# Optimization experiments

Hardware: AMD Instinct MI355X
Metric: run time of the kernel (lower is better)

The kernel has to match this reference:

```python
import jax, jax.numpy as jnp
import numpy as np

EPS = 1e-6  # mmdet bbox_overlaps eps


def _nearest_bev(boxes7):
    # boxes7: [N, 7] = (x, y, z, dx, dy, dz, yaw). LiDARInstance3DBoxes.nearest_bev:
    # limit yaw to [-pi/2, pi/2) via limit_period(yaw, 0.5, pi); if |yaw| > pi/4 swap dx/dy,
    # then return axis-aligned (x1, y1, x2, y2).
    x, y = boxes7[:, 0], boxes7[:, 1]
    dx, dy = boxes7[:, 3], boxes7[:, 4]
    yaw = boxes7[:, 6]
    pi = jnp.float32(np.pi)
    normed = jnp.abs(yaw - jnp.floor(yaw / pi + 0.5) * pi)
    swap = normed > pi / 4
    w = jnp.where(swap, dy, dx)
    h = jnp.where(swap, dx, dy)
    return jnp.stack([x - w / 2, y - h / 2, x + w / 2, y + h / 2], axis=-1)


def _pairwise_iou(b):
    # b: [N, 4] x1y1x2y2 -> [N, N] IoU (mmdet bbox_overlaps, mode='iou')
    area = (b[:, 2] - b[:, 0]) * (b[:, 3] - b[:, 1])
    lt = jnp.maximum(b[:, None, :2], b[None, :, :2])
    rb = jnp.minimum(b[:, None, 2:], b[None, :, 2:])
    wh = jnp.clip(rb - lt, 0.0)
    inter = wh[..., 0] * wh[..., 1]
    union = jnp.maximum(area[:, None] + area[None, :] - inter, EPS)
    return inter / union


def setup_inputs() -> dict:
    key = jax.random.key(0)
    k1, k2, k3, k4, k5, k6 = jax.random.split(key, 6)
    B, A, C, H, W, box_dim = 2, 2, 10, 32, 32, 7
    N = H * W * A
    scores = jax.random.normal(k1, (B, A * C, H, W), jnp.float32)
    bbox_preds = jax.random.normal(k2, (B, A * box_dim, H, W), jnp.float32)
    pp_params = jax.random.normal(k3, (B, C * 3, H, W), jnp.float32)
    centers = jax.random.uniform(k4, (B, N, 3), jnp.float32, 0.0, 50.0)
    sizes = jax.random.uniform(k5, (B, N, 3), jnp.float32, 1.0, 5.0)
    yaw = jax.random.uniform(k6, (B, N, 1), jnp.float32, -np.pi, np.pi)
    decoded = jnp.concatenate([centers, sizes, yaw], axis=-1)  # [B, N, 7]
    return {"scores": scores, "bbox_preds": bbox_preds, "pp_params": pp_params, "decoded": decoded}


def reference(scores, bbox_preds, pp_params, decoded):
    B, AC, H, W = scores.shape
    N = decoded.shape[1]
    A = N // (H * W)
    C = AC // A
    # flatten_scores: (B,A,C,H,W) -> (B,H,W,A,C) -> (B, HWA, C)
    sc_f = scores.reshape(B, A, C, H, W).transpose(0, 3, 4, 1, 2).reshape(B, N, C)
    # flatten_pp: (B,C,3,H,W) -> (B,H,W,C,3), broadcast over A -> (B, HWA, C, 3)
    pp_hw = pp_params.reshape(B, C, 3, H, W).transpose(0, 3, 4, 1, 2)  # [B,H,W,C,3]
    pp_f = jnp.broadcast_to(pp_hw[:, :, :, None, :, :], (B, H, W, A, C, 3)).reshape(B, N, C, 3)
    # per-batch BEV IoU matrices
    bev = jax.vmap(_nearest_bev)(decoded[..., :7])        # [B, N, 4]
    iou = jax.vmap(_pairwise_iou)(bev)                    # [B, N, N]
    # per-class outer-product bias + row softmax + matmul with column softmax of scores
    p0 = pp_f[..., 0]                                     # [B, N, C]
    p1 = pp_f[..., 1]                                     # [B, N, C]
    bias = p0[:, :, None, :] * p1[:, None, :, :]          # [B, N, N, C]
    weight = jax.nn.softmax(iou[..., None] + bias, axis=2)  # softmax over keys (dim=1 of NxN)
    sm_sc = jax.nn.softmax(sc_f, axis=1)                  # softmax over N per class
    new_sc = jnp.einsum('bnmc,bmc->bnc', weight, sm_sc)   # [B, N, C]
    # un-flatten back to level layout: (B,H,W,A,C) -> (B, A*C, H, W)
    out_scores = new_sc.reshape(B, H, W, A, C).transpose(0, 3, 4, 1, 2).reshape(B, A * C, H, W)
    return out_scores, bbox_preds, pp_params
```

## Files before the change

### kernel.cpp

```cpp
#include <hip/hip_runtime.h>
#include <math.h>

#define Bz 2
#define Az 2
#define Cz 10
#define HWz 1024
#define Nz 2048
#define ACHW (Az*Cz*HWz)
#define NBBOX (Bz*Az*7*HWz)
#define NPP   (Bz*Cz*3*HWz)
#define EPSf 1e-6f
#define LOG2E 1.4426950408889634f

#if __has_builtin(__builtin_amdgcn_exp2f)
#define EXP2F(x) __builtin_amdgcn_exp2f(x)
#else
#define EXP2F(x) exp2f(x)
#endif
#if __has_builtin(__builtin_amdgcn_rcpf)
#define RCPF(x) __builtin_amdgcn_rcpf(x)
#else
#define RCPF(x) (1.0f/(x))
#endif

static __device__ __forceinline__ unsigned short f2bf(float x) {
    unsigned u = __builtin_bit_cast(unsigned, x);
    unsigned r = (u + 0x7fffu + ((u >> 16) & 1u)) >> 16;
    return (unsigned short)r;
}

#if __has_builtin(__builtin_amdgcn_update_dpp)
static __device__ __forceinline__ float wred(float x) {
    int t;
    t = __builtin_amdgcn_update_dpp(0, __builtin_bit_cast(int, x), 0x111, 0xf, 0xf, true);
    x += __builtin_bit_cast(float, t);
    t = __builtin_amdgcn_update_dpp(0, __builtin_bit_cast(int, x), 0x112, 0xf, 0xf, true);
    x += __builtin_bit_cast(float, t);
    t = __builtin_amdgcn_update_dpp(0, __builtin_bit_cast(int, x), 0x114, 0xf, 0xf, true);
    x += __builtin_bit_cast(float, t);
    t = __builtin_amdgcn_update_dpp(0, __builtin_bit_cast(int, x), 0x118, 0xf, 0xf, true);
    x += __builtin_bit_cast(float, t);
    t = __builtin_amdgcn_update_dpp(0, __builtin_bit_cast(int, x), 0x142, 0xa, 0xf, true);
    x += __builtin_bit_cast(float, t);
    t = __builtin_amdgcn_update_dpp(0, __builtin_bit_cast(int, x), 0x143, 0xc, 0xf, true);
    x += __builtin_bit_cast(float, t);
    return x;
}
#define WRED_LANE 63
#else
static __device__ __forceinline__ float wred(float x) {
    for (int off = 32; off > 0; off >>= 1) x += __shfl_down(x, off);
    return x;
}
#define WRED_LANE 0
#endif

static __device__ __forceinline__ float iou_e(float nx1,float ny1,float nx2,float ny2,float ar,
                                              float mx1,float my1,float mx2,float my2,float am) {
    float xx1 = fmaxf(nx1, mx1), yy1 = fmaxf(ny1, my1);
    float xx2 = fminf(nx2, mx2), yy2 = fminf(ny2, my2);
    float iw = fmaxf(xx2 - xx1, 0.f), ih = fmaxf(yy2 - yy1, 0.f);
    float inter = iw * ih;
    float uni = fmaxf(ar + am - inter, EPSf);
    return EXP2F(inter * LOG2E * RCPF(uni));
}


__global__ __launch_bounds__(256) void k_pre(const float* __restrict__ scores,
                                             const float* __restrict__ bbox,
                                             const float* __restrict__ pp,
                                             const float* __restrict__ dec,
                                             float* __restrict__ out,
                                             float2* __restrict__ LT,
                                             float2* __restrict__ RB,
                                             uint2* __restrict__ GPQ) {
    int blk = blockIdx.x;
    int tid = threadIdx.x;
    __shared__ float red[256];

    if (blk < 240) {
        int i = blk * 256 + tid;
        if (i < NBBOX) out[Bz*ACHW + i] = bbox[i];
        if (i < NPP)   out[Bz*ACHW + NBBOX + i] = pp[i];
        return;
    }
    if (blk < 256) {
        int i = (blk - 240) * 256 + tid;
        const float* d = dec + i*7;
        float x = d[0], y = d[1], dx = d[3], dy = d[4], yaw = d[6];
        const float PI = 3.14159265358979323846f;
        float normed = fabsf(yaw - floorf(yaw/PI + 0.5f) * PI);
        bool swp = normed > PI * 0.25f;
        float w = swp ? dy : dx;
        float h = swp ? dx : dy;
        LT[i] = make_float2(x - 0.5f*w, y - 0.5f*h);
        RB[i] = make_float2(x + 0.5f*w, y + 0.5f*h);
        return;
    }
    int bc = blk - 256;
    int b = bc / Cz, c = bc % Cz;
    const float* sbase = scores + b*ACHW;
    float vals[Nz/256];
    float mx = -INFINITY;
    #pragma unroll
    for (int j = 0; j < Nz/256; j++) {
        int n = tid + j*256;
        int a = n & 1, hw = n >> 1;
        float v = sbase[(a*Cz + c)*HWz + hw];
        vals[j] = v;
        mx = fmaxf(mx, v);
    }
    red[tid] = mx; __syncthreads();
    for (int s = 128; s > 0; s >>= 1) {
        if (tid < s) red[tid] = fmaxf(red[tid], red[tid+s]);
        __syncthreads();
    }
    mx = red[0]; __syncthreads();
    float sum = 0.f;
    #pragma unroll
    for (int j = 0; j < Nz/256; j++) {
        vals[j] = EXP2F((vals[j] - mx) * LOG2E);
        sum += vals[j];
    }
    red[tid] = sum; __syncthreads();
    for (int s = 128; s > 0; s >>= 1) {
        if (tid < s) red[tid] += red[tid+s];
        __syncthreads();
    }
    float inv = 1.f / red[0];
    const float* p1base = pp + b*Cz*3*HWz + (c*3 + 1)*HWz;
    uint2* gp = GPQ + (b*Cz + c)*HWz;
    #pragma unroll
    for (int j = 0; j < Nz/256; j++) {
        __syncthreads();
        red[tid] = vals[j] * inv;
        __syncthreads();
        if (tid < 128) {
            int hm = (j << 7) + tid;
            float q0 = red[2*tid], q1 = red[2*tid + 1];
            unsigned qq = (unsigned)f2bf(q0) | ((unsigned)f2bf(q1) << 16);
            float p1 = p1base[hm] * LOG2E;
            gp[hm] = make_uint2(__builtin_bit_cast(unsigned, p1), qq);
        }
    }
}

__global__ __launch_bounds__(256) void k_main(const float4* __restrict__ LT4,
                                              const float4* __restrict__ RB4,
                                              const uint2* __restrict__ GPQ,
                                              const float* __restrict__ pp,
                                              float* __restrict__ out) {
    __shared__ float4 SB[256];
    __shared__ uint2  SPQ[Cz*128];
    int tid = threadIdx.x;
    int wave = tid >> 6, lane = tid & 63;
    int bid = blockIdx.x;
    int b = bid >> 8;
    int hn = ((bid & 255) << 2) + wave;

    const float4* LTb = LT4 + (b << 10);
    const float4* RBb = RB4 + (b << 10);
    const uint2*  PQb = GPQ + b * (Cz * HWz);

    float4 bx = LTb[hn];
    float4 by = RBb[hn];
    float ar0 = (by.x - bx.x) * (by.y - bx.y);
    float ar1 = (by.z - bx.z) * (by.w - bx.w);

    float p0[Cz];
    const float* p0base = pp + b*(Cz*3*HWz) + hn;
    #pragma unroll
    for (int c = 0; c < Cz; c++) p0[c] = p0base[c * 3 * HWz];

    float l0[Cz], l1[Cz], a0[Cz], a1[Cz];
    #pragma unroll
    for (int c = 0; c < Cz; c++) { l0[c]=0.f; l1[c]=0.f; a0[c]=0.f; a1[c]=0.f; }

    float4 rB = (tid < 128) ? LTb[tid] : RBb[tid - 128];
    uint2 rq[5];
    #pragma unroll
    for (int k = 0; k < 5; k++) {
        int u = tid + (k << 8);
        rq[k] = PQb[((u >> 7) << 10) + (u & 127)];
    }

    for (int cb = 0; cb < 8; cb++) {
        __syncthreads();
        SB[tid] = rB;
        #pragma unroll
        for (int k = 0; k < 5; k++) SPQ[tid + (k << 8)] = rq[k];
        __syncthreads();
        if (cb < 7) {
            int nb = (cb + 1) << 7;
            rB = (tid < 128) ? LTb[nb + tid] : RBb[nb + tid - 128];
            #pragma unroll
            for (int k = 0; k < 5; k++) {
                int u = tid + (k << 8);
                rq[k] = PQb[((u >> 7) << 10) + nb + (u & 127)];
            }
        }
        #pragma unroll
        for (int half = 0; half < 2; half++) {
            int hm = (half << 6) + lane;
            float4 bl = SB[hm];
            float4 br = SB[128 + hm];
            float am0 = (br.x - bl.x) * (br.y - bl.y);
            float am1 = (br.z - bl.z) * (br.w - bl.w);
            float E00 = iou_e(bx.x,bx.y,by.x,by.y,ar0, bl.x,bl.y,br.x,br.y,am0);
            float E01 = iou_e(bx.x,bx.y,by.x,by.y,ar0, bl.z,bl.w,br.z,br.w,am1);
            float E10 = iou_e(bx.z,bx.w,by.z,by.w,ar1, bl.x,bl.y,br.x,br.y,am0);
            float E11 = iou_e(bx.z,bx.w,by.z,by.w,ar1, bl.z,bl.w,br.z,br.w,am1);
            float S0 = E00 + E01, S1 = E10 + E11;
            #pragma unroll
            for (int c = 0; c < Cz; c++) {
                uint2 pq = SPQ[(c << 7) + hm];
                float p1 = __builtin_bit_cast(float, pq.x);
                float q0 = __builtin_bit_cast(float, pq.y << 16);
                float q1 = __builtin_bit_cast(float, pq.y & 0xffff0000u);
                float F = EXP2F(p0[c] * p1);
                l0[c] = fmaf(F, S0, l0[c]);
                l1[c] = fmaf(F, S1, l1[c]);
                float t0 = fmaf(E01, q1, E00 * q0);
                float t1 = fmaf(E11, q1, E10 * q0);
                a0[c] = fmaf(F, t0, a0[c]);
                a1[c] = fmaf(F, t1, a1[c]);
            }
        }
    }

    #pragma unroll
    for (int c = 0; c < Cz; c++) {
        l0[c] = wred(l0[c]); l1[c] = wred(l1[c]);
        a0[c] = wred(a0[c]); a1[c] = wred(a1[c]);
    }
    if (lane == WRED_LANE) {
        float* ob = out + b*ACHW + hn;
        #pragma unroll
        for (int c = 0; c < Cz; c++) {
            ob[c * HWz]        = a0[c] * RCPF(l0[c]);
            ob[(Cz + c) * HWz] = a1[c] * RCPF(l1[c]);
        }
    }
}

extern "C" void kernel_launch(void* const* d_in, const int* in_sizes, int n_in,
                              void* d_out, int out_size, void* d_ws, size_t ws_size,
                              hipStream_t stream) {
    const float* scores = (const float*)d_in[0];
    const float* bbox   = (const float*)d_in[1];
    const float* pp     = (const float*)d_in[2];
    const float* dec    = (const float*)d_in[3];
    float* out = (float*)d_out;

    float2* LT = (float2*)d_ws;
    float2* RB = LT + (size_t)Bz*Nz;
    uint2*  PQ = (uint2*)(RB + (size_t)Bz*Nz);

    hipLaunchKernelGGL(k_pre,  dim3(276), dim3(256), 0, stream,
                       scores, bbox, pp, dec, out, LT, RB, PQ);
    hipLaunchKernelGGL(k_main, dim3(512), dim3(256), 0, stream,
                       (const float4*)LT, (const float4*)RB, PQ, pp, out);
}
```

Measured before the change: 81.41 us.

## Split key range across two waves per row and read keys directly from global

Result: slower. 105.8 us (+30.0%).

```diff
diff --git a/kernel.cpp b/kernel.cpp
--- a/kernel.cpp
+++ b/kernel.cpp
@@ -145,18 +145,19 @@
     }
 }
 
-__global__ __launch_bounds__(256) void k_main(const float4* __restrict__ LT4,
-                                              const float4* __restrict__ RB4,
-                                              const uint2* __restrict__ GPQ,
-                                              const float* __restrict__ pp,
-                                              float* __restrict__ out) {
-    __shared__ float4 SB[256];
-    __shared__ uint2  SPQ[Cz*128];
+__global__ __launch_bounds__(256, 4) void k_main(const float4* __restrict__ LT4,
+                                                 const float4* __restrict__ RB4,
+                                                 const uint2* __restrict__ GPQ,
+                                                 const float* __restrict__ pp,
+                                                 float* __restrict__ out) {
+    __shared__ float SR[4][40];
     int tid = threadIdx.x;
     int wave = tid >> 6, lane = tid & 63;
     int bid = blockIdx.x;
-    int b = bid >> 8;
-    int hn = ((bid & 255) << 2) + wave;
+    int b = bid >> 9;
+    int blk = bid & 511;
+    int hn = (blk << 1) + (wave >> 1);
+    int mhalf = wave & 1;
 
     const float4* LTb = LT4 + (b << 10);
     const float4* RBb = RB4 + (b << 10);
@@ -176,55 +177,35 @@
     #pragma unroll
     for (int c = 0; c < Cz; c++) { l0[c]=0.f; l1[c]=0.f; a0[c]=0.f; a1[c]=0.f; }
 
-    float4 rB = (tid < 128) ? LTb[tid] : RBb[tid - 128];
-    uint2 rq[5];
-    #pragma unroll
-    for (int k = 0; k < 5; k++) {
-        int u = tid + (k << 8);
-        rq[k] = PQb[((u >> 7) << 10) + (u & 127)];
-    }
-
-    for (int cb = 0; cb < 8; cb++) {
-        __syncthreads();
-        SB[tid] = rB;
+    int hm0 = (mhalf << 9) + lane;
+    for (int it = 0; it < 8; it++) {
+        int hm = hm0 + (it << 6);
+        float4 bl = LTb[hm];
+        float4 br = RBb[hm];
+        uint2 pqv[Cz];
         #pragma unroll
-        for (int k = 0; k < 5; k++) SPQ[tid + (k << 8)] = rq[k];
-        __syncthreads();
-        if (cb < 7) {
-            int nb = (cb + 1) << 7;
-            rB = (tid < 128) ? LTb[nb + tid] : RBb[nb + tid - 128];
-            #pragma unroll
-            for (int k = 0; k < 5; k++) {
-                int u = tid + (k << 8);
-                rq[k] = PQb[((u >> 7) << 10) + nb + (u & 127)];
-            }
-        }
+        for (int c = 0; c < Cz; c++) pqv[c] = PQb[(c << 10) + hm];
+
+        float am0 = (br.x - bl.x) * (br.y - bl.y);
+        float am1 = (br.z - bl.z) * (br.w - bl.w);
+        float E00 = iou_e(bx.x,bx.y,by.x,by.y,ar0, bl.x,bl.y,br.x,br.y,am0);
+        float E01 = iou_e(bx.x,bx.y,by.x,by.y,ar0, bl.z,bl.w,br.z,br.w,am1);
+        float E10 = iou_e(bx.z,bx.w,by.z,by.w,ar1, bl.x,bl.y,br.x,br.y,am0);
+        float E11 = iou_e(bx.z,bx.w,by.z,by.w,ar1, bl.z,bl.w,br.z,br.w,am1);
+        float S0 = E00 + E01, S1 = E10 + E11;
         #pragma unroll
-        for (int half = 0; half < 2; half++) {
-            int hm = (half << 6) + lane;
-            float4 bl = SB[hm];
-            float4 br = SB[128 + hm];
-            float am0 = (br.x - bl.x) * (br.y - bl.y);
-            float am1 = (br.z - bl.z) * (br.w - bl.w);
-            float E00 = iou_e(bx.x,bx.y,by.x,by.y,ar0, bl.x,bl.y,br.x,br.y,am0);
-            float E01 = iou_e(bx.x,bx.y,by.x,by.y,ar0, bl.z,bl.w,br.z,br.w,am1);
-            float E10 = iou_e(bx.z,bx.w,by.z,by.w,ar1, bl.x,bl.y,br.x,br.y,am0);
-            float E11 = iou_e(bx.z,bx.w,by.z,by.w,ar1, bl.z,bl.w,br.z,br.w,am1);
-            float S0 = E00 + E01, S1 = E10 + E11;
-            #pragma unroll
-            for (int c = 0; c < Cz; c++) {
-                uint2 pq = SPQ[(c << 7) + hm];
-                float p1 = __builtin_bit_cast(float, pq.x);
-                float q0 = __builtin_bit_cast(float, pq.y << 16);
-                float q1 = __builtin_bit_cast(float, pq.y & 0xffff0000u);
-                float F = EXP2F(p0[c] * p1);
-                l0[c] = fmaf(F, S0, l0[c]);
-                l1[c] = fmaf(F, S1, l1[c]);
-                float t0 = fmaf(E01, q1, E00 * q0);
-                float t1 = fmaf(E11, q1, E10 * q0);
-                a0[c] = fmaf(F, t0, a0[c]);
-                a1[c] = fmaf(F, t1, a1[c]);
-            }
+        for (int c = 0; c < Cz; c++) {
+            uint2 pq = pqv[c];
+            float p1 = __builtin_bit_cast(float, pq.x);
+            float q0 = __builtin_bit_cast(float, pq.y << 16);
+            float q1 = __builtin_bit_cast(float, pq.y & 0xffff0000u);
+            float F = EXP2F(p0[c] * p1);
+            l0[c] = fmaf(F, S0, l0[c]);
+            l1[c] = fmaf(F, S1, l1[c]);
+            float t0 = fmaf(E01, q1, E00 * q0);
+            float t1 = fmaf(E11, q1, E10 * q0);
+            a0[c] = fmaf(F, t0, a0[c]);
+            a1[c] = fmaf(F, t1, a1[c]);
         }
     }
 
@@ -234,12 +215,22 @@
         a0[c] = wred(a0[c]); a1[c] = wred(a1[c]);
     }
     if (lane == WRED_LANE) {
-        float* ob = out + b*ACHW + hn;
         #pragma unroll
         for (int c = 0; c < Cz; c++) {
-            ob[c * HWz]        = a0[c] * RCPF(l0[c]);
-            ob[(Cz + c) * HWz] = a1[c] * RCPF(l1[c]);
+            SR[wave][c]      = l0[c];
+            SR[wave][10 + c] = l1[c];
+            SR[wave][20 + c] = a0[c];
+            SR[wave][30 + c] = a1[c];
         }
+    }
+    __syncthreads();
+    if (tid < 40) {
+        int p = tid / 20, rc = tid % 20;
+        int row = rc / 10, c = rc % 10;
+        int w0 = p << 1;
+        float l = SR[w0][row*10 + c] + SR[w0+1][row*10 + c];
+        float a = SR[w0][20 + row*10 + c] + SR[w0+1][20 + row*10 + c];
+        out[b*ACHW + (row*Cz + c)*HWz + (blk << 1) + p] = a * RCPF(l);
     }
 }
 
@@ -256,8 +247,8 @@
     float2* RB = LT + (size_t)Bz*Nz;
     uint2*  PQ = (uint2*)(RB + (size_t)Bz*Nz);
 
-    hipLaunchKernelGGL(k_pre,  dim3(276), dim3(256), 0, stream,
+    hipLaunchKernelGGL(k_pre,  dim3(276),  dim3(256), 0, stream,
                        scores, bbox, pp, dec, out, LT, RB, PQ);
-    hipLaunchKernelGGL(k_main, dim3(512), dim3(256), 0, stream,
+    hipLaunchKernelGGL(k_main, dim3(1024), dim3(256), 0, stream,
                        (const float4*)LT, (const float4*)RB, PQ, pp, out);
 }
```

## Split key dimension across blocks with lane-per-query layout and separate reduction kernel

Applied to the files above, without the earlier changes.

After: 85.41 us. +4.9%, slower.

```diff
diff --git a/kernel.cpp b/kernel.cpp
--- a/kernel.cpp
+++ b/kernel.cpp
@@ -29,32 +29,6 @@
     return (unsigned short)r;
 }
 
-#if __has_builtin(__builtin_amdgcn_update_dpp)
-static __device__ __forceinline__ float wred(float x) {
-    int t;
-    t = __builtin_amdgcn_update_dpp(0, __builtin_bit_cast(int, x), 0x111, 0xf, 0xf, true);
-    x += __builtin_bit_cast(float, t);
-    t = __builtin_amdgcn_update_dpp(0, __builtin_bit_cast(int, x), 0x112, 0xf, 0xf, true);
-    x += __builtin_bit_cast(float, t);
-    t = __builtin_amdgcn_update_dpp(0, __builtin_bit_cast(int, x), 0x114, 0xf, 0xf, true);
-    x += __builtin_bit_cast(float, t);
-    t = __builtin_amdgcn_update_dpp(0, __builtin_bit_cast(int, x), 0x118, 0xf, 0xf, true);
-    x += __builtin_bit_cast(float, t);
-    t = __builtin_amdgcn_update_dpp(0, __builtin_bit_cast(int, x), 0x142, 0xa, 0xf, true);
-    x += __builtin_bit_cast(float, t);
-    t = __builtin_amdgcn_update_dpp(0, __builtin_bit_cast(int, x), 0x143, 0xc, 0xf, true);
-    x += __builtin_bit_cast(float, t);
-    return x;
-}
-#define WRED_LANE 63
-#else
-static __device__ __forceinline__ float wred(float x) {
-    for (int off = 32; off > 0; off >>= 1) x += __shfl_down(x, off);
-    return x;
-}
-#define WRED_LANE 0
-#endif
-
 static __device__ __forceinline__ float iou_e(float nx1,float ny1,float nx2,float ny2,float ar,
                                               float mx1,float my1,float mx2,float my2,float am) {
     float xx1 = fmaxf(nx1, mx1), yy1 = fmaxf(ny1, my1);
@@ -73,7 +47,7 @@
                                              float* __restrict__ out,
                                              float2* __restrict__ LT,
                                              float2* __restrict__ RB,
-                                             uint2* __restrict__ GPQ) {
+                                             uint2* __restrict__ GPQ2) {
     int blk = blockIdx.x;
     int tid = threadIdx.x;
     __shared__ float red[256];
@@ -129,7 +103,7 @@
     }
     float inv = 1.f / red[0];
     const float* p1base = pp + b*Cz*3*HWz + (c*3 + 1)*HWz;
-    uint2* gp = GPQ + (b*Cz + c)*HWz;
+    uint2* gp = GPQ2 + (size_t)b*HWz*Cz;
     #pragma unroll
     for (int j = 0; j < Nz/256; j++) {
         __syncthreads();
@@ -140,33 +114,43 @@
             float q0 = red[2*tid], q1 = red[2*tid + 1];
             unsigned qq = (unsigned)f2bf(q0) | ((unsigned)f2bf(q1) << 16);
             float p1 = p1base[hm] * LOG2E;
-            gp[hm] = make_uint2(__builtin_bit_cast(unsigned, p1), qq);
+            gp[hm*Cz + c] = make_uint2(__builtin_bit_cast(unsigned, p1), qq);
         }
     }
 }
 
-__global__ __launch_bounds__(256) void k_main(const float4* __restrict__ LT4,
-                                              const float4* __restrict__ RB4,
-                                              const uint2* __restrict__ GPQ,
-                                              const float* __restrict__ pp,
-                                              float* __restrict__ out) {
-    __shared__ float4 SB[256];
-    __shared__ uint2  SPQ[Cz*128];
+__global__ __launch_bounds__(256, 2) void k_main(const float4* __restrict__ LT4,
+                                                 const float4* __restrict__ RB4,
+                                                 const uint2* __restrict__ GPQ2,
+                                                 const float* __restrict__ pp,
+                                                 float* __restrict__ P) {
+    __shared__ __align__(16) char smem[40960];
+    float4* SLT = (float4*)smem;
+    float4* SRB = SLT + 64;
+    uint2*  SPQ = (uint2*)(SRB + 64);
+    float*  RED = (float*)smem;
+
     int tid = threadIdx.x;
     int wave = tid >> 6, lane = tid & 63;
     int bid = blockIdx.x;
     int b = bid >> 8;
-    int hn = ((bid & 255) << 2) + wave;
+    int r = bid & 255;
+    int g = r >> 4, sp = r & 15;
+    int hbase = sp << 6;
 
     const float4* LTb = LT4 + (b << 10);
     const float4* RBb = RB4 + (b << 10);
-    const uint2*  PQb = GPQ + b * (Cz * HWz);
-
-    float4 bx = LTb[hn];
-    float4 by = RBb[hn];
+    const uint2*  Qb  = GPQ2 + (size_t)b*HWz*Cz + (size_t)hbase*Cz;
+
+    if (tid < 64)       SLT[tid] = LTb[hbase + tid];
+    else if (tid < 128) SRB[tid - 64] = RBb[hbase + tid - 64];
+    #pragma unroll
+    for (int i = tid; i < 640; i += 256) SPQ[i] = Qb[i];
+
+    int hn = (g << 6) + lane;
+    float4 bx = LTb[hn], by = RBb[hn];
     float ar0 = (by.x - bx.x) * (by.y - bx.y);
     float ar1 = (by.z - bx.z) * (by.w - bx.w);
-
     float p0[Cz];
     const float* p0base = pp + b*(Cz*3*HWz) + hn;
     #pragma unroll
@@ -176,70 +160,79 @@
     #pragma unroll
     for (int c = 0; c < Cz; c++) { l0[c]=0.f; l1[c]=0.f; a0[c]=0.f; a1[c]=0.f; }
 
-    float4 rB = (tid < 128) ? LTb[tid] : RBb[tid - 128];
-    uint2 rq[5];
-    #pragma unroll
-    for (int k = 0; k < 5; k++) {
-        int u = tid + (k << 8);
-        rq[k] = PQb[((u >> 7) << 10) + (u & 127)];
-    }
-
-    for (int cb = 0; cb < 8; cb++) {
-        __syncthreads();
-        SB[tid] = rB;
-        #pragma unroll
-        for (int k = 0; k < 5; k++) SPQ[tid + (k << 8)] = rq[k];
-        __syncthreads();
-        if (cb < 7) {
-            int nb = (cb + 1) << 7;
-            rB = (tid < 128) ? LTb[nb + tid] : RBb[nb + tid - 128];
-            #pragma unroll
-            for (int k = 0; k < 5; k++) {
-                int u = tid + (k << 8);
-                rq[k] = PQb[((u >> 7) << 10) + nb + (u & 127)];
-            }
-        }
-        #pragma unroll
-        for (int half = 0; half < 2; half++) {
-            int hm = (half << 6) + lane;
-            float4 bl = SB[hm];
-            float4 br = SB[128 + hm];
-            float am0 = (br.x - bl.x) * (br.y - bl.y);
-            float am1 = (br.z - bl.z) * (br.w - bl.w);
-            float E00 = iou_e(bx.x,bx.y,by.x,by.y,ar0, bl.x,bl.y,br.x,br.y,am0);
-            float E01 = iou_e(bx.x,bx.y,by.x,by.y,ar0, bl.z,bl.w,br.z,br.w,am1);
-            float E10 = iou_e(bx.z,bx.w,by.z,by.w,ar1, bl.x,bl.y,br.x,br.y,am0);
-            float E11 = iou_e(bx.z,bx.w,by.z,by.w,ar1, bl.z,bl.w,br.z,br.w,am1);
-            float S0 = E00 + E01, S1 = E10 + E11;
-            #pragma unroll
-            for (int c = 0; c < Cz; c++) {
-                uint2 pq = SPQ[(c << 7) + hm];
-                float p1 = __builtin_bit_cast(float, pq.x);
-                float q0 = __builtin_bit_cast(float, pq.y << 16);
-                float q1 = __builtin_bit_cast(float, pq.y & 0xffff0000u);
-                float F = EXP2F(p0[c] * p1);
-                l0[c] = fmaf(F, S0, l0[c]);
-                l1[c] = fmaf(F, S1, l1[c]);
-                float t0 = fmaf(E01, q1, E00 * q0);
-                float t1 = fmaf(E11, q1, E10 * q0);
-                a0[c] = fmaf(F, t0, a0[c]);
-                a1[c] = fmaf(F, t1, a1[c]);
-            }
-        }
-    }
-
-    #pragma unroll
-    for (int c = 0; c < Cz; c++) {
-        l0[c] = wred(l0[c]); l1[c] = wred(l1[c]);
-        a0[c] = wred(a0[c]); a1[c] = wred(a1[c]);
-    }
-    if (lane == WRED_LANE) {
-        float* ob = out + b*ACHW + hn;
+    __syncthreads();
+
+    int j0 = wave << 4;
+    #pragma unroll 4
+    for (int i = 0; i < 16; i++) {
+        int j = j0 + i;
+        float4 bl = SLT[j];
+        float4 br = SRB[j];
+        float am0 = (br.x - bl.x) * (br.y - bl.y);
+        float am1 = (br.z - bl.z) * (br.w - bl.w);
+        float E00 = iou_e(bx.x,bx.y,by.x,by.y,ar0, bl.x,bl.y,br.x,br.y,am0);
+        float E01 = iou_e(bx.x,bx.y,by.x,by.y,ar0, bl.z,bl.w,br.z,br.w,am1);
+        float E10 = iou_e(bx.z,bx.w,by.z,by.w,ar1, bl.x,bl.y,br.x,br.y,am0);
+        float E11 = iou_e(bx.z,bx.w,by.z,by.w,ar1, bl.z,bl.w,br.z,br.w,am1);
+        float S0 = E00 + E01, S1 = E10 + E11;
+        const uint2* pqrow = SPQ + j*Cz;
         #pragma unroll
         for (int c = 0; c < Cz; c++) {
-            ob[c * HWz]        = a0[c] * RCPF(l0[c]);
-            ob[(Cz + c) * HWz] = a1[c] * RCPF(l1[c]);
+            uint2 pq = pqrow[c];
+            float p1 = __builtin_bit_cast(float, pq.x);
+            float q0 = __builtin_bit_cast(float, pq.y << 16);
+            float q1 = __builtin_bit_cast(float, pq.y & 0xffff0000u);
+            float F = EXP2F(p0[c] * p1);
+            l0[c] = fmaf(F, S0, l0[c]);
+            l1[c] = fmaf(F, S1, l1[c]);
+            float t0 = fmaf(E01, q1, E00 * q0);
+            float t1 = fmaf(E11, q1, E10 * q0);
+            a0[c] = fmaf(F, t0, a0[c]);
+            a1[c] = fmaf(F, t1, a1[c]);
         }
+    }
+
+    __syncthreads();
+    float* rw = RED + (wave*64 + lane)*40;
+    #pragma unroll
+    for (int c = 0; c < Cz; c++) {
+        rw[c]      = l0[c];
+        rw[10 + c] = l1[c];
+        rw[20 + c] = a0[c];
+        rw[30 + c] = a1[c];
+    }
+    __syncthreads();
+
+    int vg = tid >> 6, ln = tid & 63;
+    float* Pb = P + (size_t)bid * 2560;
+    #pragma unroll
+    for (int k = 0; k < 10; k++) {
+        int v = vg + (k << 2);
+        float s = RED[(0*64+ln)*40 + v] + RED[(1*64+ln)*40 + v]
+                + RED[(2*64+ln)*40 + v] + RED[(3*64+ln)*40 + v];
+        Pb[v*64 + ln] = s;
+    }
+}
+
+__global__ __launch_bounds__(256) void k_red(const float* __restrict__ P,
+                                             float* __restrict__ out) {
+    int bg = blockIdx.x;
+    int b = bg >> 4, g = bg & 15;
+    const float* Pb = P + (size_t)bg * 16 * 2560;
+    int tid = threadIdx.x;
+    #pragma unroll
+    for (int k = 0; k < 5; k++) {
+        int pos = tid + (k << 8);
+        int v2 = pos >> 6, ln = pos & 63;
+        float l = 0.f, a = 0.f;
+        #pragma unroll
+        for (int sp = 0; sp < 16; sp++) {
+            const float* q = Pb + sp*2560;
+            l += q[pos];
+            a += q[1280 + pos];
+        }
+        int row = v2 / 10, c = v2 % 10;
+        out[b*ACHW + (row*Cz + c)*HWz + (g << 6) + ln] = a * RCPF(l);
     }
 }
 
@@ -255,9 +248,11 @@
     float2* LT = (float2*)d_ws;
     float2* RB = LT + (size_t)Bz*Nz;
     uint2*  PQ = (uint2*)(RB + (size_t)Bz*Nz);
+    float*  P  = (float*)(PQ + (size_t)Bz*HWz*Cz);
 
     hipLaunchKernelGGL(k_pre,  dim3(276), dim3(256), 0, stream,
                        scores, bbox, pp, dec, out, LT, RB, PQ);
     hipLaunchKernelGGL(k_main, dim3(512), dim3(256), 0, stream,
-                       (const float4*)LT, (const float4*)RB, PQ, pp, out);
-}
+                       (const float4*)LT, (const float4*)RB, PQ, pp, P);
+    hipLaunchKernelGGL(k_red,  dim3(32),  dim3(256), 0, stream, P, out);
+}
```
